# Performance work log

Hardware: AMD Instinct MI355X
Metric: run time of the kernel (lower is better)

Reference implementation:

```python
import jax, jax.numpy as jnp
import numpy as np

N_IN, N_HID, N_OUT = 200, 256, 2
BN_EPS = 1e-5


def _mlp(x, W1, b1, W2, b2):
    # two-layer MLP with ELU activations (dropout prob = 0.0 -> omitted)
    h = jax.nn.elu(x @ W1 + b1)
    return jax.nn.elu(h @ W2 + b2)


def _batch_norm(x, gamma, beta):
    # torch BatchNorm1d in training mode over flattened (B*E) rows, biased variance
    m = x.mean(axis=(0, 1))
    v = x.var(axis=(0, 1))
    return (x - m) * jax.lax.rsqrt(v + BN_EPS) * gamma + beta


def setup_inputs() -> dict:
    key = jax.random.key(0)
    ks = jax.random.split(key, 12)
    B, N, T, D = 32, 100, 50, 4
    inputs = jax.random.normal(ks[0], (B, N, T, D), dtype=jnp.float32)
    # one-hot receiver/sender matrices over all N*(N-1) ordered off-diagonal pairs
    idx = np.array([(i, j) for i in range(N) for j in range(N) if i != j])
    eye = np.eye(N, dtype=np.float32)
    rel_rec = jnp.asarray(eye[idx[:, 0]])   # [E, N]
    rel_send = jnp.asarray(eye[idx[:, 1]])  # [E, N]

    def lin(k, fi, fo):  # xavier_normal weight
        std = float(np.sqrt(2.0 / (fi + fo)))
        return jax.random.normal(k, (fi, fo), dtype=jnp.float32) * std

    b = lambda n: jnp.full((n,), 0.1, dtype=jnp.float32)
    return dict(
        inputs=inputs, rel_rec=rel_rec, rel_send=rel_send,
        mlp1_W1=lin(ks[1], N_IN, N_HID), mlp1_b1=b(N_HID),
        mlp1_W2=lin(ks[2], N_HID, N_HID), mlp1_b2=b(N_HID),
        mlp2_W1=lin(ks[3], 2 * N_HID, N_HID), mlp2_b1=b(N_HID),
        mlp2_W2=lin(ks[4], N_HID, N_HID), mlp2_b2=b(N_HID),
        mlp3_W1=lin(ks[5], N_HID, N_HID), mlp3_b1=b(N_HID),
        mlp3_W2=lin(ks[6], N_HID, N_HID), mlp3_b2=b(N_HID),
        mlp4_W1=lin(ks[7], 3 * N_HID, N_HID), mlp4_b1=b(N_HID),
        mlp4_W2=lin(ks[8], N_HID, N_HID), mlp4_b2=b(N_HID),
        mlp4_bn_gamma=jnp.ones((N_HID,), jnp.float32),
        mlp4_bn_beta=jnp.zeros((N_HID,), jnp.float32),
        fc_W=lin(ks[9], N_HID, N_OUT), fc_b=b(N_OUT),
    )


def reference(inputs, rel_rec, rel_send,
              mlp1_W1, mlp1_b1, mlp1_W2, mlp1_b2,
              mlp2_W1, mlp2_b1, mlp2_W2, mlp2_b2,
              mlp3_W1, mlp3_b1, mlp3_W2, mlp3_b2,
              mlp4_W1, mlp4_b1, mlp4_W2, mlp4_b2,
              mlp4_bn_gamma, mlp4_bn_beta, fc_W, fc_b):
    B, N = inputs.shape[0], inputs.shape[1]
    x = inputs.reshape(B, N, -1)                       # [B, N, T*D]
    x = _mlp(x, mlp1_W1, mlp1_b1, mlp1_W2, mlp1_b2)     # [B, N, H]

    def node2edge(h):
        recv = jnp.einsum('en,bnh->beh', rel_rec, h)
        send = jnp.einsum('en,bnh->beh', rel_send, h)
        return jnp.concatenate([send, recv], axis=2)    # [B, E, 2H]

    x = node2edge(x)
    x = _mlp(x, mlp2_W1, mlp2_b1, mlp2_W2, mlp2_b2)     # [B, E, H]
    x_skip = x
    # factor=True branch
    incoming = jnp.einsum('en,beh->bnh', rel_rec, x) / x.shape[1]  # edge2node, /N per code
    x = _mlp(incoming, mlp3_W1, mlp3_b1, mlp3_W2, mlp3_b2)
    x = node2edge(x)                                    # [B, E, 2H]
    x = jnp.concatenate([x, x_skip], axis=2)            # [B, E, 3H]
    x = _mlp(x, mlp4_W1, mlp4_b1, mlp4_W2, mlp4_b2)
    x = _batch_norm(x, mlp4_bn_gamma, mlp4_bn_beta)
    return x @ fc_W + fc_b                              # [B, E, n_out]
```

## Files before the change

kernel.cpp:

```cpp
#include <hip/hip_runtime.h>
#include <math.h>


typedef unsigned short ushort_t;
typedef __bf16 bf16x8 __attribute__((ext_vector_type(8)));
typedef float  f32x4  __attribute__((ext_vector_type(4)));

#define E_EDGES 9900
#define NNODE   100
#define HID     256
#define M_BIG   316800
#define M_SMALL 3200
#define NBLK2   (M_BIG / 128)

__device__ __forceinline__ float bf2f(ushort_t u) {
    union { unsigned int i; float f; } v; v.i = ((unsigned int)u) << 16; return v.f;
}
__device__ __forceinline__ ushort_t f2bf(float f) {
    union { float f; unsigned int i; } v; v.f = f;
    return (ushort_t)((v.i + 0x7fffu + ((v.i >> 16) & 1u)) >> 16);
}
__device__ __forceinline__ float elu_f(float x) {
    return x > 0.f ? x : (__expf(x) - 1.f);
}

__global__ __launch_bounds__(256)
void wcvt_all(const float* __restrict__ s0, const float* __restrict__ s1,
              const float* __restrict__ s2, const float* __restrict__ s3,
              const float* __restrict__ s4, const float* __restrict__ s5,
              const float* __restrict__ s6, const float* __restrict__ s7,
              ushort_t* d0, ushort_t* d1, ushort_t* d2, ushort_t* d3,
              ushort_t* d4, ushort_t* d5, ushort_t* d6, ushort_t* d7)
{
    int bid = blockIdx.x;
    const float* S; ushort_t* D; int Kd, Kr, t;
    if      (bid < 16)  { S = s0; D = d0; Kd = 256; Kr = 200; t = bid; }
    else if (bid < 32)  { S = s1; D = d1; Kd = 256; Kr = 256; t = bid - 16; }
    else if (bid < 64)  { S = s2; D = d2; Kd = 512; Kr = 512; t = bid - 32; }
    else if (bid < 80)  { S = s3; D = d3; Kd = 256; Kr = 256; t = bid - 64; }
    else if (bid < 96)  { S = s4; D = d4; Kd = 256; Kr = 256; t = bid - 80; }
    else if (bid < 112) { S = s5; D = d5; Kd = 256; Kr = 256; t = bid - 96; }
    else if (bid < 160) { S = s6; D = d6; Kd = 768; Kr = 768; t = bid - 112; }
    else                { S = s7; D = d7; Kd = 256; Kr = 256; t = bid - 160; }
    int k0 = (t >> 2) * 64, c0 = (t & 3) * 64;
    __shared__ float Sh[64][65];
    int tid = threadIdx.x;
    #pragma unroll
    for (int i = 0; i < 16; ++i) {
        int idx = tid + i * 256;
        int kk = idx >> 6, cc = idx & 63;
        Sh[kk][cc] = (k0 + kk < Kr) ? S[(size_t)(k0 + kk) * 256 + c0 + cc] : 0.f;
    }
    __syncthreads();
    int col = tid & 63;
    int kb  = (tid >> 6) * 16;
    ushort_t* dst = D + (size_t)(c0 + col) * Kd + k0 + kb;
    #pragma unroll
    for (int jj = 0; jj < 4; ++jj) {
        ushort4 u;
        u.x = f2bf(Sh[kb + 4 * jj + 0][col]);
        u.y = f2bf(Sh[kb + 4 * jj + 1][col]);
        u.z = f2bf(Sh[kb + 4 * jj + 2][col]);
        u.w = f2bf(Sh[kb + 4 * jj + 3][col]);
        *(ushort4*)(dst + 4 * jj) = u;
    }
}

template<int XF32>
__global__ __launch_bounds__(256, 2)
void small_mfma(const float* __restrict__ Xf, const ushort_t* __restrict__ Xb,
                int Kreal, int kcN, float xscale, int act, int nb1,
                const ushort_t* __restrict__ WTa, int wsa,
                const float* __restrict__ ba, ushort_t* __restrict__ Ya,
                const ushort_t* __restrict__ WTb, int wsb,
                const float* __restrict__ bb, ushort_t* __restrict__ Yb)
{
    __shared__ ushort_t Xs[32][264];
    int bid = blockIdx.x;
    const ushort_t* WT; int wstr; const float* bias; ushort_t* Y;
    if (bid < nb1) { WT = WTa; wstr = wsa; bias = ba; Y = Ya; }
    else           { bid -= nb1; WT = WTb; wstr = wsb; bias = bb; Y = Yb; }
    const int tid = threadIdx.x;
    const int w = tid >> 6;
    const int l = tid & 63;
    const int ln15 = l & 15;
    const int q = l >> 4;
    const int klane = 8 * q;
    const int Rbase = bid * 32;

    {
        int row = tid >> 3, seg = tid & 7;
        if (seg < kcN) {
            ushort_t tmp[32];
            if (XF32) {
                const float* src = Xf + (size_t)(Rbase + row) * Kreal + seg * 32;
                #pragma unroll
                for (int u = 0; u < 32; ++u)
                    tmp[u] = (seg * 32 + u < Kreal) ? f2bf(src[u]) : (ushort_t)0;
            } else {
                const ushort_t* src = Xb + (size_t)(Rbase + row) * 256 + seg * 32;
                #pragma unroll
                for (int u = 0; u < 4; ++u)
                    *(uint4*)&tmp[u * 8] = *(const uint4*)(src + u * 8);
            }
            #pragma unroll
            for (int u = 0; u < 4; ++u)
                *(uint4*)&Xs[row][seg * 32 + u * 8] = *(uint4*)&tmp[u * 8];
        }
    }
    __syncthreads();

    f32x4 acc[2][4];
    #pragma unroll
    for (int r = 0; r < 2; ++r)
        #pragma unroll
        for (int c = 0; c < 4; ++c)
            acc[r][c][0] = acc[r][c][1] = acc[r][c][2] = acc[r][c][3] = 0.f;
    int wch[4];
    #pragma unroll
    for (int c = 0; c < 4; ++c) wch[c] = (w * 64 + 16 * c + ln15) * wstr;

    {
        bf16x8 wf0[4];
        #pragma unroll
        for (int c = 0; c < 4; ++c)
            wf0[c] = *(const bf16x8*)(WT + wch[c] + klane);
        for (int kc = 0; kc < kcN; ++kc) {
            bf16x8 wf1[4];
            if (kc + 1 < kcN) {
                #pragma unroll
                for (int c = 0; c < 4; ++c)
                    wf1[c] = *(const bf16x8*)(WT + wch[c] + (kc + 1) * 32 + klane);
            }
            bf16x8 af[2];
            #pragma unroll
            for (int r = 0; r < 2; ++r)
                af[r] = *(const bf16x8*)&Xs[16 * r + ln15][kc * 32 + klane];
            #pragma unroll
            for (int r = 0; r < 2; ++r)
                #pragma unroll
                for (int c = 0; c < 4; ++c)
                    acc[r][c] = __builtin_amdgcn_mfma_f32_16x16x32_bf16(wf0[c], af[r], acc[r][c], 0, 0, 0);
            #pragma unroll
            for (int c = 0; c < 4; ++c) wf0[c] = wf1[c];
        }
    }
    __syncthreads();

    #pragma unroll
    for (int c = 0; c < 4; ++c) {
        float4 bv = bias ? *(const float4*)&bias[w * 64 + 16 * c + 4 * q]
                         : make_float4(0.f, 0.f, 0.f, 0.f);
        #pragma unroll
        for (int r = 0; r < 2; ++r) {
            float o0 = acc[r][c][0] * xscale + bv.x;
            float o1 = acc[r][c][1] * xscale + bv.y;
            float o2 = acc[r][c][2] * xscale + bv.z;
            float o3 = acc[r][c][3] * xscale + bv.w;
            if (act) { o0 = elu_f(o0); o1 = elu_f(o1); o2 = elu_f(o2); o3 = elu_f(o3); }
            ushort4 u;
            u.x = f2bf(o0); u.y = f2bf(o1); u.z = f2bf(o2); u.w = f2bf(o3);
            *(ushort4*)&Xs[16 * r + ln15][w * 64 + 16 * c + 4 * q] = u;
        }
    }
    __syncthreads();
    #pragma unroll
    for (int m = 0; m < 4; ++m) {
        int ch = tid + m * 256;
        int row = ch >> 5;
        int o = (ch & 31) * 8;
        *(uint4*)&Y[(size_t)(Rbase + row) * 256 + o] = *(const uint4*)&Xs[row][o];
    }
}

__global__ __launch_bounds__(256, 2)
void edge_mlp2(const ushort_t* __restrict__ Pb, const ushort_t* __restrict__ Qb,
               const ushort_t* __restrict__ W2T,
               const float* __restrict__ b2,
               ushort_t* __restrict__ Y, float* __restrict__ aux)
{
    __shared__ ushort_t As[128][264];
    const int tid = threadIdx.x;
    const int w = tid >> 6;
    const int l = tid & 63;
    const int ln15 = l & 15;
    const int q = l >> 4;
    const int klane = 8 * q;
    const int Rbase = blockIdx.x * 128;

    for (int h = 0; h < 2; ++h) {
        int row = (tid >> 2) + 64 * h;
        int R = Rbase + row;
        int b = R / E_EDGES;
        int e = R - b * E_EDGES;
        int i = e / 99;
        int k = e - 99 * i;
        int j = k + (k >= i ? 1 : 0);
        const ushort_t* prow = Pb + (size_t)(b * NNODE + j) * HID;
        const ushort_t* qrow = Qb + (size_t)(b * NNODE + i) * HID;
        int off = (tid & 3) * 8;
        uint4 pv[8], qv[8];
        #pragma unroll
        for (int u = 0; u < 8; ++u) {
            int o = off + u * 32;
            pv[u] = *(const uint4*)(prow + o);
            qv[u] = *(const uint4*)(qrow + o);
        }
        #pragma unroll
        for (int u = 0; u < 8; ++u) {
            int o = off + u * 32;
            union { uint4 v; ushort_t s[8]; } pu, qu, hu;
            pu.v = pv[u]; qu.v = qv[u];
            #pragma unroll
            for (int x = 0; x < 8; ++x)
                hu.s[x] = f2bf(elu_f(bf2f(pu.s[x]) + bf2f(qu.s[x])));
            *(uint4*)&As[row][o] = hu.v;
        }
    }
    __syncthreads();

    f32x4 acc[8][4];
    #pragma unroll
    for (int r = 0; r < 8; ++r)
        #pragma unroll
        for (int c = 0; c < 4; ++c)
            acc[r][c][0] = acc[r][c][1] = acc[r][c][2] = acc[r][c][3] = 0.f;
    int wch[4];
    #pragma unroll
    for (int c = 0; c < 4; ++c) wch[c] = (w * 64 + 16 * c + ln15) * 256;
    {
        bf16x8 wf0[4];
        #pragma unroll
        for (int c = 0; c < 4; ++c)
            wf0[c] = *(const bf16x8*)(W2T + wch[c] + klane);
        #pragma unroll
        for (int kc = 0; kc < 8; ++kc) {
            bf16x8 wf1[4];
            if (kc < 7) {
                #pragma unroll
                for (int c = 0; c < 4; ++c)
                    wf1[c] = *(const bf16x8*)(W2T + wch[c] + (kc + 1) * 32 + klane);
            }
            bf16x8 af[8];
            #pragma unroll
            for (int r = 0; r < 8; ++r)
                af[r] = *(const bf16x8*)&As[16 * r + ln15][kc * 32 + klane];
            #pragma unroll
            for (int r = 0; r < 8; ++r)
                #pragma unroll
                for (int c = 0; c < 4; ++c)
                    acc[r][c] = __builtin_amdgcn_mfma_f32_16x16x32_bf16(wf0[c], af[r], acc[r][c], 0, 0, 0);
            #pragma unroll
            for (int c = 0; c < 4; ++c) wf0[c] = wf1[c];
        }
    }
    __syncthreads();

    #pragma unroll
    for (int c = 0; c < 4; ++c) {
        float4 bv = *(const float4*)&b2[w * 64 + 16 * c + 4 * q];
        #pragma unroll
        for (int r = 0; r < 8; ++r) {
            ushort4 u;
            u.x = f2bf(elu_f(acc[r][c][0] + bv.x));
            u.y = f2bf(elu_f(acc[r][c][1] + bv.y));
            u.z = f2bf(elu_f(acc[r][c][2] + bv.z));
            u.w = f2bf(elu_f(acc[r][c][3] + bv.w));
            *(ushort4*)&As[16 * r + ln15][w * 64 + 16 * c + 4 * q] = u;
        }
    }
    __syncthreads();

    #pragma unroll
    for (int m = 0; m < 16; ++m) {
        int ch = tid + m * 256;
        int row = ch >> 5;
        int o = (ch & 31) * 8;
        *(uint4*)&Y[((size_t)(Rbase + row)) * 256 + o] = *(const uint4*)&As[row][o];
    }

    if (tid < 64) {
        int c4 = tid * 4;
        int bn = Rbase / 99;
        int left = 99 - (Rbase - bn * 99);
        float s[4] = {0.f, 0.f, 0.f, 0.f};
        for (int r = 0; r < 128; ++r) {
            union { ushort4 v; ushort_t e[4]; } u;
            u.v = *(const ushort4*)&As[r][c4];
            #pragma unroll
            for (int g = 0; g < 4; ++g) s[g] += bf2f(u.e[g]);
            if (--left == 0) {
                #pragma unroll
                for (int g = 0; g < 4; ++g) {
                    atomicAdd(&aux[(size_t)bn * 256 + c4 + g], s[g]);
                    s[g] = 0.f;
                }
                ++bn; left = 99;
            }
        }
        #pragma unroll
        for (int g = 0; g < 4; ++g)
            atomicAdd(&aux[(size_t)bn * 256 + c4 + g], s[g]);
    }
}

__global__ __launch_bounds__(256, 2)
void edge_mlp4(const ushort_t* __restrict__ Pb, const ushort_t* __restrict__ Qb,
               const ushort_t* __restrict__ X2,
               const ushort_t* __restrict__ WaT, int wsA,
               const ushort_t* __restrict__ WbT, int wsB,
               const float* __restrict__ b2,
               ushort_t* __restrict__ Y, ushort_t* __restrict__ pstat)
{
    __shared__ ushort_t As[128][264];
    const int tid = threadIdx.x;
    const int w = tid >> 6;
    const int l = tid & 63;
    const int ln15 = l & 15;
    const int q = l >> 4;
    const int klane = 8 * q;
    const int Rbase = blockIdx.x * 128;

    #pragma unroll
    for (int h = 0; h < 2; ++h) {
        int row = (tid >> 2) + 64 * h;
        const ushort_t* xrow = X2 + (size_t)(Rbase + row) * 256;
        int off = (tid & 3) * 8;
        uint4 xv[8];
        #pragma unroll
        for (int u = 0; u < 8; ++u) xv[u] = *(const uint4*)(xrow + off + u * 32);
        #pragma unroll
        for (int u = 0; u < 8; ++u) *(uint4*)&As[row][off + u * 32] = xv[u];
    }

    int oP[8], oQ[8];
    #pragma unroll
    for (int r = 0; r < 8; ++r) {
        int R = Rbase + 16 * r + ln15;
        int b = R / E_EDGES;
        int e = R - b * E_EDGES;
        int i = e / 99;
        int k = e - 99 * i;
        int j = k + (k >= i ? 1 : 0);
        oP[r] = (b * NNODE + j) * HID;
        oQ[r] = (b * NNODE + i) * HID;
    }
    __syncthreads();

    f32x4 acc[8][4];
    int wchA[4], wchB[4];
    #pragma unroll
    for (int c = 0; c < 4; ++c) {
        wchA[c] = (w * 64 + 16 * c + ln15) * wsA;
        wchB[c] = (w * 64 + 16 * c + ln15) * wsB;
    }

    #pragma unroll
    for (int r = 0; r < 8; ++r)
        #pragma unroll
        for (int c = 0; c < 4; ++c)
            acc[r][c][0] = acc[r][c][1] = acc[r][c][2] = acc[r][c][3] = 0.f;
    {
        bf16x8 wf0[4];
        #pragma unroll
        for (int c = 0; c < 4; ++c)
            wf0[c] = *(const bf16x8*)(WaT + wchA[c] + klane);
        #pragma unroll
        for (int kc = 0; kc < 8; ++kc) {
            bf16x8 wf1[4];
            if (kc < 7) {
                #pragma unroll
                for (int c = 0; c < 4; ++c)
                    wf1[c] = *(const bf16x8*)(WaT + wchA[c] + (kc + 1) * 32 + klane);
            }
            bf16x8 af[8];
            #pragma unroll
            for (int r = 0; r < 8; ++r)
                af[r] = *(const bf16x8*)&As[16 * r + ln15][kc * 32 + klane];
            #pragma unroll
            for (int r = 0; r < 8; ++r)
                #pragma unroll
                for (int c = 0; c < 4; ++c)
                    acc[r][c] = __builtin_amdgcn_mfma_f32_16x16x32_bf16(wf0[c], af[r], acc[r][c], 0, 0, 0);
            #pragma unroll
            for (int c = 0; c < 4; ++c) wf0[c] = wf1[c];
        }
    }
    __syncthreads();

    #pragma unroll
    for (int c = 0; c < 4; ++c) {
        int ch = w * 64 + 16 * c + 4 * q;
        ushort4 pv[8], qv[8];
        #pragma unroll
        for (int r = 0; r < 8; ++r) {
            pv[r] = *(const ushort4*)(Pb + oP[r] + ch);
            qv[r] = *(const ushort4*)(Qb + oQ[r] + ch);
        }
        #pragma unroll
        for (int r = 0; r < 8; ++r) {
            union { ushort4 v; ushort_t s[4]; } pu, qu;
            pu.v = pv[r]; qu.v = qv[r];
            ushort4 u;
            u.x = f2bf(elu_f(acc[r][c][0] + bf2f(pu.s[0]) + bf2f(qu.s[0])));
            u.y = f2bf(elu_f(acc[r][c][1] + bf2f(pu.s[1]) + bf2f(qu.s[1])));
            u.z = f2bf(elu_f(acc[r][c][2] + bf2f(pu.s[2]) + bf2f(qu.s[2])));
            u.w = f2bf(elu_f(acc[r][c][3] + bf2f(pu.s[3]) + bf2f(qu.s[3])));
            *(ushort4*)&As[16 * r + ln15][ch] = u;
        }
    }
    __syncthreads();

    #pragma unroll
    for (int r = 0; r < 8; ++r)
        #pragma unroll
        for (int c = 0; c < 4; ++c)
            acc[r][c][0] = acc[r][c][1] = acc[r][c][2] = acc[r][c][3] = 0.f;
    {
        bf16x8 wf0[4];
        #pragma unroll
        for (int c = 0; c < 4; ++c)
            wf0[c] = *(const bf16x8*)(WbT + wchB[c] + klane);
        #pragma unroll
        for (int kc = 0; kc < 8; ++kc) {
            bf16x8 wf1[4];
            if (kc < 7) {
                #pragma unroll
                for (int c = 0; c < 4; ++c)
                    wf1[c] = *(const bf16x8*)(WbT + wchB[c] + (kc + 1) * 32 + klane);
            }
            bf16x8 af[8];
            #pragma unroll
            for (int r = 0; r < 8; ++r)
                af[r] = *(const bf16x8*)&As[16 * r + ln15][kc * 32 + klane];
            #pragma unroll
            for (int r = 0; r < 8; ++r)
                #pragma unroll
                for (int c = 0; c < 4; ++c)
                    acc[r][c] = __builtin_amdgcn_mfma_f32_16x16x32_bf16(wf0[c], af[r], acc[r][c], 0, 0, 0);
            #pragma unroll
            for (int c = 0; c < 4; ++c) wf0[c] = wf1[c];
        }
    }
    __syncthreads();

    #pragma unroll
    for (int c = 0; c < 4; ++c) {
        float4 bv = *(const float4*)&b2[w * 64 + 16 * c + 4 * q];
        #pragma unroll
        for (int r = 0; r < 8; ++r) {
            ushort4 u;
            u.x = f2bf(elu_f(acc[r][c][0] + bv.x));
            u.y = f2bf(elu_f(acc[r][c][1] + bv.y));
            u.z = f2bf(elu_f(acc[r][c][2] + bv.z));
            u.w = f2bf(elu_f(acc[r][c][3] + bv.w));
            *(ushort4*)&As[16 * r + ln15][w * 64 + 16 * c + 4 * q] = u;
        }
    }
    __syncthreads();

    #pragma unroll
    for (int m = 0; m < 16; ++m) {
        int ch = tid + m * 256;
        int row = ch >> 5;
        int o = (ch & 31) * 8;
        *(uint4*)&Y[((size_t)(Rbase + row)) * 256 + o] = *(const uint4*)&As[row][o];
    }

    if (tid < 64) {
        int c4 = tid * 4;
        float s[4] = {0.f, 0.f, 0.f, 0.f};
        float qq[4] = {0.f, 0.f, 0.f, 0.f};
        for (int r = 0; r < 128; ++r) {
            union { ushort4 v; ushort_t e[4]; } u;
            u.v = *(const ushort4*)&As[r][c4];
            #pragma unroll
            for (int g = 0; g < 4; ++g) {
                float v = bf2f(u.e[g]);
                s[g] += v;
                qq[g] = fmaf(v, v, qq[g]);
            }
        }
        size_t base = (size_t)blockIdx.x * 512;
        ushort4 us, uq;
        us.x = f2bf(s[0]);  us.y = f2bf(s[1]);  us.z = f2bf(s[2]);  us.w = f2bf(s[3]);
        uq.x = f2bf(qq[0]); uq.y = f2bf(qq[1]); uq.z = f2bf(qq[2]); uq.w = f2bf(qq[3]);
        *(ushort4*)&pstat[base + c4]       = us;
        *(ushort4*)&pstat[base + 256 + c4] = uq;
    }
}

__global__ __launch_bounds__(256)
void reduce_stats(const ushort_t* __restrict__ pstat, float* __restrict__ stats)
{
    int c = threadIdx.x;
    float s = 0.f, q = 0.f;
    for (int b = blockIdx.x; b < NBLK2; b += 64) {
        size_t base = (size_t)b * 512;
        s += bf2f(pstat[base + c]);
        q += bf2f(pstat[base + 256 + c]);
    }
    atomicAdd(&stats[c], s);
    atomicAdd(&stats[256 + c], q);
}

__global__ __launch_bounds__(256)
void fold_kernel(const float* __restrict__ stats,
                 const float* __restrict__ gamma, const float* __restrict__ beta,
                 const float* __restrict__ fcW, const float* __restrict__ fcb,
                 float* __restrict__ fold)
{
    __shared__ float red0[256], red1[256];
    int c = threadIdx.x;
    float mean  = stats[c] * (1.f / M_BIG);
    float var   = stats[256 + c] * (1.f / M_BIG) - mean * mean;
    float inv   = rsqrtf(var + 1e-5f);
    float scale = inv * gamma[c];
    float sh    = beta[c] - mean * scale;
    float w0 = fcW[c * 2 + 0], w1 = fcW[c * 2 + 1];
    fold[c * 2 + 0] = scale * w0;
    fold[c * 2 + 1] = scale * w1;
    red0[c] = sh * w0;
    red1[c] = sh * w1;
    __syncthreads();
    for (int off = 128; off > 0; off >>= 1) {
        if (c < off) { red0[c] += red0[c + off]; red1[c] += red1[c + off]; }
        __syncthreads();
    }
    if (c == 0) {
        fold[512] = red0[0] + fcb[0];
        fold[513] = red1[0] + fcb[1];
    }
}

__global__ __launch_bounds__(256)
void final_kernel(const ushort_t* __restrict__ x4, const float* __restrict__ fold,
                  float* __restrict__ out)
{
    int tid  = threadIdx.x;
    int l32  = tid & 31;
    int g    = tid >> 5;
    int R = blockIdx.x * 8 + g;
    int c0 = l32 * 8;
    union { uint4 qv; ushort_t s[8]; } u;
    u.qv = *(const uint4*)(x4 + (size_t)R * 256 + c0);
    float a0 = 0.f, a1 = 0.f;
    #pragma unroll
    for (int j = 0; j < 8; ++j) {
        float v = bf2f(u.s[j]);
        a0 = fmaf(v, fold[(c0 + j) * 2 + 0], a0);
        a1 = fmaf(v, fold[(c0 + j) * 2 + 1], a1);
    }
    #pragma unroll
    for (int off = 16; off > 0; off >>= 1) {
        a0 += __shfl_down(a0, off);
        a1 += __shfl_down(a1, off);
    }
    if (l32 == 0) {
        out[(size_t)R * 2 + 0] = a0 + fold[512];
        out[(size_t)R * 2 + 1] = a1 + fold[513];
    }
}

extern "C" void kernel_launch(void* const* d_in, const int* in_sizes, int n_in,
                              void* d_out, int out_size, void* d_ws, size_t ws_size,
                              hipStream_t stream)
{
    (void)in_sizes; (void)n_in; (void)out_size; (void)ws_size;

    const float* inputs = (const float*)d_in[0];
    const float* m1W1 = (const float*)d_in[3];
    const float* m1b1 = (const float*)d_in[4];
    const float* m1W2 = (const float*)d_in[5];
    const float* m1b2 = (const float*)d_in[6];
    const float* m2W1 = (const float*)d_in[7];
    const float* m2b1 = (const float*)d_in[8];
    const float* m2W2 = (const float*)d_in[9];
    const float* m2b2 = (const float*)d_in[10];
    const float* m3W1 = (const float*)d_in[11];
    const float* m3b1 = (const float*)d_in[12];
    const float* m3W2 = (const float*)d_in[13];
    const float* m3b2 = (const float*)d_in[14];
    const float* m4W1 = (const float*)d_in[15];
    const float* m4b1 = (const float*)d_in[16];
    const float* m4W2 = (const float*)d_in[17];
    const float* m4b2 = (const float*)d_in[18];
    const float* gamma = (const float*)d_in[19];
    const float* beta  = (const float*)d_in[20];
    const float* fcW   = (const float*)d_in[21];
    const float* fcb   = (const float*)d_in[22];
    float* out = (float*)d_out;

    char* ws = (char*)d_ws;
    const size_t BIGB = (size_t)M_BIG * 256 * 2;
    const size_t HB   = (size_t)M_SMALL * 256 * 2;
    const size_t SM4  = (size_t)M_SMALL * 256 * 4;
    ushort_t* bigX     = (ushort_t*)ws;
    ushort_t* ha       = (ushort_t*)(ws + BIGB);
    ushort_t* hb       = (ushort_t*)(ws + BIGB + HB);
    ushort_t* pstat    = (ushort_t*)(ws + BIGB);
    float*    incoming = (float*)(ws + BIGB + 2 * HB);
    ushort_t* Pbuf     = (ushort_t*)(ws + BIGB + 2 * HB + SM4);
    ushort_t* Qbuf     = (ushort_t*)(ws + BIGB + 3 * HB + SM4);
    float*    stats    = (float*)(ws + BIGB + 4 * HB + SM4);
    float*    fold     = stats + 512;
    ushort_t* w1t      = (ushort_t*)(ws + BIGB + 4 * HB + SM4 + 8192);
    ushort_t* w1bt     = w1t  + 256 * 256;
    ushort_t* w2pt     = w1bt + 256 * 256;
    ushort_t* w2t      = w2pt + 256 * 512;
    ushort_t* w3at     = w2t  + 256 * 256;
    ushort_t* w3bt     = w3at + 256 * 256;
    ushort_t* w4pt     = w3bt + 256 * 256;
    ushort_t* w4bt     = w4pt + 256 * 768;

    hipMemsetAsync(stats, 0, 2048, stream);
    hipMemsetAsync(incoming, 0, SM4, stream);

    dim3 blk(256);
    wcvt_all<<<176, blk, 0, stream>>>(m1W1, m1W2, m2W1, m2W2, m3W1, m3W2, m4W1, m4W2,
                                      w1t, w1bt, w2pt, w2t, w3at, w3bt, w4pt, w4bt);
    small_mfma<1><<<100, blk, 0, stream>>>(inputs, nullptr, 200, 7, 1.f, 1, 100,
                                           w1t, 256, m1b1, ha,
                                           nullptr, 0, nullptr, nullptr);
    small_mfma<0><<<100, blk, 0, stream>>>(nullptr, ha, 256, 8, 1.f, 1, 100,
                                           w1bt, 256, m1b2, hb,
                                           nullptr, 0, nullptr, nullptr);
    small_mfma<0><<<200, blk, 0, stream>>>(nullptr, hb, 256, 8, 1.f, 0, 100,
                                           w2pt, 512, m2b1, Pbuf,
                                           w2pt + 256, 512, nullptr, Qbuf);
    edge_mlp2<<<NBLK2, blk, 0, stream>>>(Pbuf, Qbuf, w2t, m2b2, bigX, incoming);
    small_mfma<1><<<100, blk, 0, stream>>>(incoming, nullptr, 256, 8, 1.f / 9900.f, 1, 100,
                                           w3at, 256, m3b1, ha,
                                           nullptr, 0, nullptr, nullptr);
    small_mfma<0><<<100, blk, 0, stream>>>(nullptr, ha, 256, 8, 1.f, 1, 100,
                                           w3bt, 256, m3b2, hb,
                                           nullptr, 0, nullptr, nullptr);
    small_mfma<0><<<200, blk, 0, stream>>>(nullptr, hb, 256, 8, 1.f, 0, 100,
                                           w4pt, 768, m4b1, Pbuf,
                                           w4pt + 256, 768, nullptr, Qbuf);
    edge_mlp4<<<NBLK2, blk, 0, stream>>>(Pbuf, Qbuf, bigX,
                                         w4pt + 512, 768, w4bt, 256,
                                         m4b2, bigX, pstat);
    reduce_stats<<<64, blk, 0, stream>>>(pstat, stats);
    fold_kernel<<<1, blk, 0, stream>>>(stats, gamma, beta, fcW, fcb, fold);
    final_kernel<<<M_BIG / 8, blk, 0, stream>>>(bigX, fold, out);
}
```

Before: 518.7 us.

## Fuse node-MLP chain into one kernel and prefetch P/Q gathers in edge_mlp4

Replaces the three small_mfma launches per node stage (layer1, layer2, P/Q projection) with a single mlp_pq kernel that keeps intermediates in two shared-memory tiles, removing launches and global round-trips for the small 3200-row activations. The xscale is now applied to inputs before bf16 conversion instead of after the GEMM. Separately, edge_mlp4 issues the gathered P/Q loads earlier and software-pipelines them one channel group ahead of the epilogue to hide gather latency, at the cost of more registers. The fused kernel runs only 100 blocks doing four sequential GEMMs, so it has little parallelism.

Result: no change. 520.1 us (+0.3%).

```diff
diff --git a/kernel.cpp b/kernel.cpp
--- a/kernel.cpp
+++ b/kernel.cpp
@@ -66,110 +66,128 @@
     }
 }
 
-template<int XF32>
-__global__ __launch_bounds__(256, 2)
-void small_mfma(const float* __restrict__ Xf, const ushort_t* __restrict__ Xb,
-                int Kreal, int kcN, float xscale, int act, int nb1,
-                const ushort_t* __restrict__ WTa, int wsa,
-                const float* __restrict__ ba, ushort_t* __restrict__ Ya,
-                const ushort_t* __restrict__ WTb, int wsb,
-                const float* __restrict__ bb, ushort_t* __restrict__ Yb)
-{
-    __shared__ ushort_t Xs[32][264];
-    int bid = blockIdx.x;
-    const ushort_t* WT; int wstr; const float* bias; ushort_t* Y;
-    if (bid < nb1) { WT = WTa; wstr = wsa; bias = ba; Y = Ya; }
-    else           { bid -= nb1; WT = WTb; wstr = wsb; bias = bb; Y = Yb; }
+__device__ __forceinline__ void gemm32(const ushort_t S[32][264],
+                                       const ushort_t* __restrict__ WT,
+                                       int wstr, int kcn,
+                                       int w, int ln15, int klane,
+                                       f32x4 acc[2][4])
+{
+    #pragma unroll
+    for (int r = 0; r < 2; ++r)
+        #pragma unroll
+        for (int c = 0; c < 4; ++c)
+            acc[r][c][0] = acc[r][c][1] = acc[r][c][2] = acc[r][c][3] = 0.f;
+    int wch[4];
+    #pragma unroll
+    for (int c = 0; c < 4; ++c) wch[c] = (w * 64 + 16 * c + ln15) * wstr;
+    bf16x8 wf0[4];
+    #pragma unroll
+    for (int c = 0; c < 4; ++c)
+        wf0[c] = *(const bf16x8*)(WT + wch[c] + klane);
+    for (int kc = 0; kc < kcn; ++kc) {
+        bf16x8 wf1[4];
+        if (kc + 1 < kcn) {
+            #pragma unroll
+            for (int c = 0; c < 4; ++c)
+                wf1[c] = *(const bf16x8*)(WT + wch[c] + (kc + 1) * 32 + klane);
+        }
+        bf16x8 af[2];
+        #pragma unroll
+        for (int r = 0; r < 2; ++r)
+            af[r] = *(const bf16x8*)&S[16 * r + ln15][kc * 32 + klane];
+        #pragma unroll
+        for (int r = 0; r < 2; ++r)
+            #pragma unroll
+            for (int c = 0; c < 4; ++c)
+                acc[r][c] = __builtin_amdgcn_mfma_f32_16x16x32_bf16(wf0[c], af[r], acc[r][c], 0, 0, 0);
+        #pragma unroll
+        for (int c = 0; c < 4; ++c) wf0[c] = wf1[c];
+    }
+}
+
+__device__ __forceinline__ void park32(ushort_t D[32][264], f32x4 acc[2][4],
+                                       const float* __restrict__ bias,
+                                       int act, int w, int ln15, int q)
+{
+    #pragma unroll
+    for (int c = 0; c < 4; ++c) {
+        float4 bv = bias ? *(const float4*)&bias[w * 64 + 16 * c + 4 * q]
+                         : make_float4(0.f, 0.f, 0.f, 0.f);
+        #pragma unroll
+        for (int r = 0; r < 2; ++r) {
+            float o0 = acc[r][c][0] + bv.x;
+            float o1 = acc[r][c][1] + bv.y;
+            float o2 = acc[r][c][2] + bv.z;
+            float o3 = acc[r][c][3] + bv.w;
+            if (act) { o0 = elu_f(o0); o1 = elu_f(o1); o2 = elu_f(o2); o3 = elu_f(o3); }
+            ushort4 u;
+            u.x = f2bf(o0); u.y = f2bf(o1); u.z = f2bf(o2); u.w = f2bf(o3);
+            *(ushort4*)&D[16 * r + ln15][w * 64 + 16 * c + 4 * q] = u;
+        }
+    }
+}
+
+__global__ __launch_bounds__(256, 4)
+void mlp_pq(const float* __restrict__ Xf, int Kreal, int kcN, float xscale,
+            const ushort_t* __restrict__ W1T, const float* __restrict__ b1,
+            const ushort_t* __restrict__ W2T, const float* __restrict__ b2,
+            const ushort_t* __restrict__ WPT, int wsPQ,
+            const float* __restrict__ bP, ushort_t* __restrict__ Pout,
+            const ushort_t* __restrict__ WQT, ushort_t* __restrict__ Qout)
+{
+    __shared__ ushort_t Abuf[32][264];
+    __shared__ ushort_t Bbuf[32][264];
     const int tid = threadIdx.x;
     const int w = tid >> 6;
     const int l = tid & 63;
     const int ln15 = l & 15;
     const int q = l >> 4;
     const int klane = 8 * q;
-    const int Rbase = bid * 32;
+    const int Rbase = blockIdx.x * 32;
 
     {
         int row = tid >> 3, seg = tid & 7;
         if (seg < kcN) {
             ushort_t tmp[32];
-            if (XF32) {
-                const float* src = Xf + (size_t)(Rbase + row) * Kreal + seg * 32;
-                #pragma unroll
-                for (int u = 0; u < 32; ++u)
-                    tmp[u] = (seg * 32 + u < Kreal) ? f2bf(src[u]) : (ushort_t)0;
-            } else {
-                const ushort_t* src = Xb + (size_t)(Rbase + row) * 256 + seg * 32;
-                #pragma unroll
-                for (int u = 0; u < 4; ++u)
-                    *(uint4*)&tmp[u * 8] = *(const uint4*)(src + u * 8);
-            }
+            const float* src = Xf + (size_t)(Rbase + row) * Kreal + seg * 32;
+            #pragma unroll
+            for (int u = 0; u < 32; ++u)
+                tmp[u] = (seg * 32 + u < Kreal) ? f2bf(src[u] * xscale) : (ushort_t)0;
             #pragma unroll
             for (int u = 0; u < 4; ++u)
-                *(uint4*)&Xs[row][seg * 32 + u * 8] = *(uint4*)&tmp[u * 8];
+                *(uint4*)&Abuf[row][seg * 32 + u * 8] = *(uint4*)&tmp[u * 8];
         }
     }
     __syncthreads();
 
     f32x4 acc[2][4];
-    #pragma unroll
-    for (int r = 0; r < 2; ++r)
-        #pragma unroll
-        for (int c = 0; c < 4; ++c)
-            acc[r][c][0] = acc[r][c][1] = acc[r][c][2] = acc[r][c][3] = 0.f;
-    int wch[4];
-    #pragma unroll
-    for (int c = 0; c < 4; ++c) wch[c] = (w * 64 + 16 * c + ln15) * wstr;
-
-    {
-        bf16x8 wf0[4];
-        #pragma unroll
-        for (int c = 0; c < 4; ++c)
-            wf0[c] = *(const bf16x8*)(WT + wch[c] + klane);
-        for (int kc = 0; kc < kcN; ++kc) {
-            bf16x8 wf1[4];
-            if (kc + 1 < kcN) {
-                #pragma unroll
-                for (int c = 0; c < 4; ++c)
-                    wf1[c] = *(const bf16x8*)(WT + wch[c] + (kc + 1) * 32 + klane);
-            }
-            bf16x8 af[2];
-            #pragma unroll
-            for (int r = 0; r < 2; ++r)
-                af[r] = *(const bf16x8*)&Xs[16 * r + ln15][kc * 32 + klane];
-            #pragma unroll
-            for (int r = 0; r < 2; ++r)
-                #pragma unroll
-                for (int c = 0; c < 4; ++c)
-                    acc[r][c] = __builtin_amdgcn_mfma_f32_16x16x32_bf16(wf0[c], af[r], acc[r][c], 0, 0, 0);
-            #pragma unroll
-            for (int c = 0; c < 4; ++c) wf0[c] = wf1[c];
-        }
-    }
-    __syncthreads();
-
-    #pragma unroll
-    for (int c = 0; c < 4; ++c) {
-        float4 bv = bias ? *(const float4*)&bias[w * 64 + 16 * c + 4 * q]
-                         : make_float4(0.f, 0.f, 0.f, 0.f);
-        #pragma unroll
-        for (int r = 0; r < 2; ++r) {
-            float o0 = acc[r][c][0] * xscale + bv.x;
-            float o1 = acc[r][c][1] * xscale + bv.y;
-            float o2 = acc[r][c][2] * xscale + bv.z;
-            float o3 = acc[r][c][3] * xscale + bv.w;
-            if (act) { o0 = elu_f(o0); o1 = elu_f(o1); o2 = elu_f(o2); o3 = elu_f(o3); }
-            ushort4 u;
-            u.x = f2bf(o0); u.y = f2bf(o1); u.z = f2bf(o2); u.w = f2bf(o3);
-            *(ushort4*)&Xs[16 * r + ln15][w * 64 + 16 * c + 4 * q] = u;
-        }
-    }
-    __syncthreads();
+    gemm32(Abuf, W1T, 256, kcN, w, ln15, klane, acc);
+    park32(Bbuf, acc, b1, 1, w, ln15, q);
+    __syncthreads();
+    gemm32(Bbuf, W2T, 256, 8, w, ln15, klane, acc);
+    park32(Abuf, acc, b2, 1, w, ln15, q);
+    __syncthreads();
+    gemm32(Abuf, WPT, wsPQ, 8, w, ln15, klane, acc);
+    park32(Bbuf, acc, bP, 0, w, ln15, q);
+    __syncthreads();
+    f32x4 acq[2][4];
+    gemm32(Abuf, WQT, wsPQ, 8, w, ln15, klane, acq);
     #pragma unroll
     for (int m = 0; m < 4; ++m) {
         int ch = tid + m * 256;
         int row = ch >> 5;
         int o = (ch & 31) * 8;
-        *(uint4*)&Y[(size_t)(Rbase + row) * 256 + o] = *(const uint4*)&Xs[row][o];
+        *(uint4*)&Pout[(size_t)(Rbase + row) * 256 + o] = *(const uint4*)&Bbuf[row][o];
+    }
+    __syncthreads();
+    park32(Bbuf, acq, nullptr, 0, w, ln15, q);
+    __syncthreads();
+    #pragma unroll
+    for (int m = 0; m < 4; ++m) {
+        int ch = tid + m * 256;
+        int row = ch >> 5;
+        int o = (ch & 31) * 8;
+        *(uint4*)&Qout[(size_t)(Rbase + row) * 256 + o] = *(const uint4*)&Bbuf[row][o];
     }
 }
 
@@ -321,16 +339,14 @@
     const int klane = 8 * q;
     const int Rbase = blockIdx.x * 128;
 
+    uint4 xv[2][8];
     #pragma unroll
     for (int h = 0; h < 2; ++h) {
         int row = (tid >> 2) + 64 * h;
         const ushort_t* xrow = X2 + (size_t)(Rbase + row) * 256;
         int off = (tid & 3) * 8;
-        uint4 xv[8];
-        #pragma unroll
-        for (int u = 0; u < 8; ++u) xv[u] = *(const uint4*)(xrow + off + u * 32);
-        #pragma unroll
-        for (int u = 0; u < 8; ++u) *(uint4*)&As[row][off + u * 32] = xv[u];
+        #pragma unroll
+        for (int u = 0; u < 8; ++u) xv[h][u] = *(const uint4*)(xrow + off + u * 32);
     }
 
     int oP[8], oQ[8];
@@ -345,6 +361,23 @@
         oP[r] = (b * NNODE + j) * HID;
         oQ[r] = (b * NNODE + i) * HID;
     }
+    ushort4 pv0[8], qv0[8];
+    {
+        int ch0 = w * 64 + 4 * q;
+        #pragma unroll
+        for (int r = 0; r < 8; ++r) {
+            pv0[r] = *(const ushort4*)(Pb + oP[r] + ch0);
+            qv0[r] = *(const ushort4*)(Qb + oQ[r] + ch0);
+        }
+    }
+
+    #pragma unroll
+    for (int h = 0; h < 2; ++h) {
+        int row = (tid >> 2) + 64 * h;
+        int off = (tid & 3) * 8;
+        #pragma unroll
+        for (int u = 0; u < 8; ++u) *(uint4*)&As[row][off + u * 32] = xv[h][u];
+    }
     __syncthreads();
 
     f32x4 acc[8][4];
@@ -390,17 +423,20 @@
 
     #pragma unroll
     for (int c = 0; c < 4; ++c) {
+        ushort4 pv1[8], qv1[8];
+        if (c < 3) {
+            int chn = w * 64 + 16 * (c + 1) + 4 * q;
+            #pragma unroll
+            for (int r = 0; r < 8; ++r) {
+                pv1[r] = *(const ushort4*)(Pb + oP[r] + chn);
+                qv1[r] = *(const ushort4*)(Qb + oQ[r] + chn);
+            }
+        }
         int ch = w * 64 + 16 * c + 4 * q;
-        ushort4 pv[8], qv[8];
-        #pragma unroll
-        for (int r = 0; r < 8; ++r) {
-            pv[r] = *(const ushort4*)(Pb + oP[r] + ch);
-            qv[r] = *(const ushort4*)(Qb + oQ[r] + ch);
-        }
         #pragma unroll
         for (int r = 0; r < 8; ++r) {
             union { ushort4 v; ushort_t s[4]; } pu, qu;
-            pu.v = pv[r]; qu.v = qv[r];
+            pu.v = pv0[r]; qu.v = qv0[r];
             ushort4 u;
             u.x = f2bf(elu_f(acc[r][c][0] + bf2f(pu.s[0]) + bf2f(qu.s[0])));
             u.y = f2bf(elu_f(acc[r][c][1] + bf2f(pu.s[1]) + bf2f(qu.s[1])));
@@ -408,6 +444,8 @@
             u.w = f2bf(elu_f(acc[r][c][3] + bf2f(pu.s[3]) + bf2f(qu.s[3])));
             *(ushort4*)&As[16 * r + ln15][ch] = u;
         }
+        #pragma unroll
+        for (int r = 0; r < 8; ++r) { pv0[r] = pv1[r]; qv0[r] = qv1[r]; }
     }
     __syncthreads();
 
@@ -596,8 +634,6 @@
     const size_t HB   = (size_t)M_SMALL * 256 * 2;
     const size_t SM4  = (size_t)M_SMALL * 256 * 4;
     ushort_t* bigX     = (ushort_t*)ws;
-    ushort_t* ha       = (ushort_t*)(ws + BIGB);
-    ushort_t* hb       = (ushort_t*)(ws + BIGB + HB);
     ushort_t* pstat    = (ushort_t*)(ws + BIGB);
     float*    incoming = (float*)(ws + BIGB + 2 * HB);
     ushort_t* Pbuf     = (ushort_t*)(ws + BIGB + 2 * HB + SM4);
@@ -619,25 +655,15 @@
     dim3 blk(256);
     wcvt_all<<<176, blk, 0, stream>>>(m1W1, m1W2, m2W1, m2W2, m3W1, m3W2, m4W1, m4W2,
                                       w1t, w1bt, w2pt, w2t, w3at, w3bt, w4pt, w4bt);
-    small_mfma<1><<<100, blk, 0, stream>>>(inputs, nullptr, 200, 7, 1.f, 1, 100,
-                                           w1t, 256, m1b1, ha,
-                                           nullptr, 0, nullptr, nullptr);
-    small_mfma<0><<<100, blk, 0, stream>>>(nullptr, ha, 256, 8, 1.f, 1, 100,
-                                           w1bt, 256, m1b2, hb,
-                                           nullptr, 0, nullptr, nullptr);
-    small_mfma<0><<<200, blk, 0, stream>>>(nullptr, hb, 256, 8, 1.f, 0, 100,
-                                           w2pt, 512, m2b1, Pbuf,
-                                           w2pt + 256, 512, nullptr, Qbuf);
+    mlp_pq<<<100, blk, 0, stream>>>(inputs, 200, 7, 1.f,
+                                    w1t, m1b1, w1bt, m1b2,
+                                    w2pt, 512, m2b1, Pbuf,
+                                    w2pt + 256, Qbuf);
     edge_mlp2<<<NBLK2, blk, 0, stream>>>(Pbuf, Qbuf, w2t, m2b2, bigX, incoming);
-    small_mfma<1><<<100, blk, 0, stream>>>(incoming, nullptr, 256, 8, 1.f / 9900.f, 1, 100,
-                                           w3at, 256, m3b1, ha,
-                                           nullptr, 0, nullptr, nullptr);
-    small_mfma<0><<<100, blk, 0, stream>>>(nullptr, ha, 256, 8, 1.f, 1, 100,
-                                           w3bt, 256, m3b2, hb,
-                                           nullptr, 0, nullptr, nullptr);
-    small_mfma<0><<<200, blk, 0, stream>>>(nullptr, hb, 256, 8, 1.f, 0, 100,
-                                           w4pt, 768, m4b1, Pbuf,
-                                           w4pt + 256, 768, nullptr, Qbuf);
+    mlp_pq<<<100, blk, 0, stream>>>(incoming, 256, 8, 1.f / 9900.f,
+                                    w3at, m3b1, w3bt, m3b2,
+                                    w4pt, 768, m4b1, Pbuf,
+                                    w4pt + 256, Qbuf);
     edge_mlp4<<<NBLK2, blk, 0, stream>>>(Pbuf, Qbuf, bigX,
                                          w4pt + 512, 768, w4bt, 256,
                                          m4b2, bigX, pstat);
```
